# Kernel optimization log

Measured on AMD Instinct MI355X. Metric: run time of the kernel, lower is better.

The kernel has to match this reference:

```python
import jax, jax.numpy as jnp
import numpy as np

NEG_SLOPE = 0.2


def setup_inputs() -> dict:
    key = jax.random.key(0)
    ks = jax.random.split(key, 12)
    Nm, Na, E, Din, H, D = 50000, 50000, 400000, 128, 8, 32
    return {
        "master_feats": jax.random.normal(ks[0], (Nm, Din), jnp.float32),
        "attn_feats0": jax.random.normal(ks[1], (Na, Din), jnp.float32),
        "attn_feats1": jax.random.normal(ks[2], (Na, Din), jnp.float32),
        "src0": jax.random.randint(ks[3], (E,), 0, Na, jnp.int32),
        "dst0": jax.random.randint(ks[4], (E,), 0, Nm, jnp.int32),
        "src1": jax.random.randint(ks[5], (E,), 0, Na, jnp.int32),
        "dst1": jax.random.randint(ks[6], (E,), 0, Nm, jnp.int32),
        "W_master": jax.random.normal(ks[7], (Din, H * D), jnp.float32) * 0.08,
        "W0": jax.random.normal(ks[8], (Din, H * D), jnp.float32) * 0.08,
        "W1": jax.random.normal(ks[9], (Din, H * D), jnp.float32) * 0.08,
        "attn_l": jax.random.normal(ks[10], (H, D), jnp.float32) * 0.1,
        "attn_r": jax.random.normal(ks[11], (H, D), jnp.float32) * 0.1,
    }


def reference(master_feats, attn_feats0, attn_feats1, src0, dst0, src1, dst1,
              W_master, W0, W1, attn_l, attn_r):
    Nm = master_feats.shape[0]
    H, D = attn_l.shape

    # Per-node-type linear projections (no bias) + attention logits.
    ft_m = (master_feats @ W_master).reshape(Nm, H, D)        # [Nm,H,D]
    er = jnp.einsum("nhd,hd->nh", ft_m, attn_r)               # [Nm,H]

    def proj(feats, W):
        ft = (feats @ W).reshape(feats.shape[0], H, D)
        el = jnp.einsum("nhd,hd->nh", ft, attn_l)
        return ft, el

    ft0, el0 = proj(attn_feats0, W0)
    ft1, el1 = proj(attn_feats1, W1)

    lrelu = lambda x: jnp.where(x >= 0, x, NEG_SLOPE * x)
    e0 = lrelu(el0[src0] + er[dst0])                          # [E0,H]
    e1 = lrelu(el1[src1] + er[dst1])                          # [E1,H]

    # Heterograph edge softmax: normalize over ALL incoming edges of each
    # master node, regardless of source node type (subtract dst-max for
    # stability; mathematically identical to the conditional path in source).
    dst = jnp.concatenate([dst0, dst1])
    e = jnp.concatenate([e0, e1], axis=0)                     # [E0+E1,H]
    emax = jax.ops.segment_max(e, dst, num_segments=Nm)
    emax = jnp.where(jnp.isfinite(emax), emax, 0.0)           # nodes w/o edges
    ee = jnp.exp(e - emax[dst])
    esum = jax.ops.segment_sum(ee, dst, num_segments=Nm)
    a = ee / esum[dst]                                        # [E0+E1,H]

    # u_mul_e + sum aggregation onto master nodes.
    E0 = src0.shape[0]
    msg = jnp.concatenate(
        [ft0[src0] * a[:E0, :, None], ft1[src1] * a[E0:, :, None]], axis=0
    )                                                         # [E,H,D]
    rst = jax.ops.segment_sum(msg, dst, num_segments=Nm)      # [Nm,H,D]
    return rst
```

## Files before the change

kernel.cpp:

```cpp
#include <hip/hip_runtime.h>
#include <cstdint>
#include <cstddef>

#define NEG_SLOPE 0.2f

typedef __attribute__((ext_vector_type(8))) short short8;
typedef __attribute__((ext_vector_type(4))) float f32x4;

static __device__ __forceinline__ unsigned short f2bf(float x) {
  uint32_t u = __float_as_uint(x);
  uint32_t r = (u + 0x7FFFu + ((u >> 16) & 1u)) >> 16;
  return (unsigned short)r;
}
static __device__ __forceinline__ float bf2f(unsigned short b) {
  return __uint_as_float(((uint32_t)b) << 16);
}

__global__ void wt_kernel(const float* __restrict__ W0, const float* __restrict__ W1,
                          const float* __restrict__ W2,
                          unsigned short* __restrict__ T0, unsigned short* __restrict__ T1,
                          unsigned short* __restrict__ T2) {
  const float* W = (blockIdx.y == 0) ? W0 : (blockIdx.y == 1) ? W1 : W2;
  unsigned short* T = (blockIdx.y == 0) ? T0 : (blockIdx.y == 1) ? T1 : T2;
  int c = blockIdx.x * 2 + (threadIdx.x >> 7);
  int k = threadIdx.x & 127;
  T[c * 128 + k] = f2bf(W[k * 256 + c]);
}

__global__ __launch_bounds__(256)
void proj_mfma_kernel(const float* __restrict__ fm, const float* __restrict__ fa0,
                      const float* __restrict__ fa1,
                      const unsigned short* __restrict__ Wtm,
                      const unsigned short* __restrict__ Wt0,
                      const unsigned short* __restrict__ Wt1,
                      const float* __restrict__ attn_l, const float* __restrict__ attn_r,
                      int Nm, int Na0, int Na1,
                      unsigned short* __restrict__ ft_all, float* __restrict__ el_all,
                      float* __restrict__ er) {
  const int z = blockIdx.z;
  const float* feats = (z == 0) ? fm : (z == 1) ? fa0 : fa1;
  const unsigned short* Wt = (z == 0) ? Wtm : (z == 1) ? Wt0 : Wt1;
  const float* av = (z == 0) ? attn_r : attn_l;
  const int N = (z == 0) ? Nm : (z == 1) ? Na0 : Na1;
  unsigned short* ft_out = (z == 0) ? nullptr
                         : (z == 1) ? ft_all : ft_all + (size_t)Na0 * 256;
  float* el_out = (z == 0) ? er : (z == 1) ? el_all : el_all + (size_t)Na0 * 8;

  const int rb = blockIdx.x * 64;
  if (rb >= N) return;

  __shared__ unsigned short As[64 * 128];
  const int t = threadIdx.x;
  const int wid = t >> 6, lane = t & 63;
  const int l15 = lane & 15, l4 = lane >> 4;
  const int cbw = wid * 64;
  const int head0 = cbw >> 5;

  short8 bf[4][4];
  #pragma unroll
  for (int nf = 0; nf < 4; ++nf) {
    const unsigned short* wp = &Wt[(size_t)(cbw + nf * 16 + l15) * 128];
    #pragma unroll
    for (int kb = 0; kb < 4; ++kb)
      bf[kb][nf] = *(const short8*)(wp + kb * 32 + l4 * 8);
  }

  #pragma unroll
  for (int it = 0; it < 8; ++it) {
    int i = it * 256 + t;
    int r = i >> 5, kc = (i & 31) << 2;
    float4 f = make_float4(0.f, 0.f, 0.f, 0.f);
    if (rb + r < N) f = *(const float4*)(&feats[(size_t)(rb + r) * 128 + kc]);
    ushort4 u;
    u.x = f2bf(f.x); u.y = f2bf(f.y); u.z = f2bf(f.z); u.w = f2bf(f.w);
    uint32_t byte = ((uint32_t)(r * 256 + kc * 2)) ^ ((uint32_t)((r & 7) << 4));
    *(ushort4*)((char*)As + byte) = u;
  }
  __syncthreads();

  f32x4 acc[4][4];
  #pragma unroll
  for (int a = 0; a < 4; ++a)
    #pragma unroll
    for (int b = 0; b < 4; ++b)
      acc[a][b] = (f32x4){0.f, 0.f, 0.f, 0.f};

  #pragma unroll
  for (int kb = 0; kb < 4; ++kb) {
    short8 af[4];
    #pragma unroll
    for (int mf = 0; mf < 4; ++mf) {
      int row = mf * 16 + l15;
      uint32_t byte = ((uint32_t)(row * 256 + kb * 64 + l4 * 16)) ^ ((uint32_t)((row & 7) << 4));
      af[mf] = *(const short8*)((const char*)As + byte);
    }
    #pragma unroll
    for (int mf = 0; mf < 4; ++mf)
      #pragma unroll
      for (int nf = 0; nf < 4; ++nf)
        acc[mf][nf] = __builtin_amdgcn_mfma_f32_16x16x32_bf16(
            bf[kb][nf], af[mf], acc[mf][nf], 0, 0, 0);
  }

  float avf[4][4];
  #pragma unroll
  for (int nf = 0; nf < 4; ++nf)
    #pragma unroll
    for (int reg = 0; reg < 4; ++reg)
      avf[nf][reg] = av[(head0 + (nf >> 1)) * 32 + (nf & 1) * 16 + l4 * 4 + reg];

  #pragma unroll
  for (int mf = 0; mf < 4; ++mf) {
    int node = rb + mf * 16 + l15;
    bool ok = node < N;
    if (ft_out != nullptr && ok) {
      size_t base = (size_t)node * 256 + cbw + l4 * 4;
      #pragma unroll
      for (int nf = 0; nf < 4; ++nf) {
        ushort4 u;
        u.x = f2bf(acc[mf][nf][0]); u.y = f2bf(acc[mf][nf][1]);
        u.z = f2bf(acc[mf][nf][2]); u.w = f2bf(acc[mf][nf][3]);
        *(ushort4*)(&ft_out[base + nf * 16]) = u;
      }
    }
    #pragma unroll
    for (int hh = 0; hh < 2; ++hh) {
      float p = 0.f;
      #pragma unroll
      for (int reg = 0; reg < 4; ++reg) {
        p = fmaf(acc[mf][2 * hh][reg], avf[2 * hh][reg], p);
        p = fmaf(acc[mf][2 * hh + 1][reg], avf[2 * hh + 1][reg], p);
      }
      p += __shfl_xor(p, 16);
      p += __shfl_xor(p, 32);
      if (ok && l4 == 0)
        el_out[(size_t)node * 8 + head0 + hh] = p;
    }
  }
}

__global__ void count_deg_kernel(const int* __restrict__ dst0, int E0,
                                 const int* __restrict__ dst1, int E1,
                                 int* __restrict__ deg) {
  int E = E0 + E1;
  for (int i = blockIdx.x * blockDim.x + threadIdx.x; i < E;
       i += gridDim.x * blockDim.x) {
    int d = (i < E0) ? dst0[i] : dst1[i - E0];
    atomicAdd(&deg[d], 1);
  }
}

__global__ __launch_bounds__(1024)
void block_reduce_kernel(const int* __restrict__ deg, int* __restrict__ partial, int n) {
  __shared__ int wsum[16];
  const int t = threadIdx.x;
  int idx = blockIdx.x * 1024 + t;
  int v = (idx < n) ? deg[idx] : 0;
  #pragma unroll
  for (int off = 1; off < 64; off <<= 1) v += __shfl_xor(v, off);
  if ((t & 63) == 0) wsum[t >> 6] = v;
  __syncthreads();
  if (t < 16) {
    int x = wsum[t];
    #pragma unroll
    for (int off = 1; off < 16; off <<= 1) x += __shfl_xor(x, off);
    if (t == 0) partial[blockIdx.x] = x;
  }
}

__global__ __launch_bounds__(64)
void partial_scan_kernel(const int* __restrict__ partial, int* __restrict__ base,
                         int nb, int* __restrict__ offs, int n) {
  const int t = threadIdx.x;
  int v = (t < nb) ? partial[t] : 0;
  int incl = v;
  #pragma unroll
  for (int off = 1; off < 64; off <<= 1) {
    int x = __shfl_up(incl, off);
    if (t >= off) incl += x;
  }
  if (t < nb) base[t] = incl - v;
  if (t == nb - 1) offs[n] = incl;
}

__global__ __launch_bounds__(1024)
void apply_scan_kernel(const int* __restrict__ deg, const int* __restrict__ base,
                       int* __restrict__ offs, int* __restrict__ cursor, int n) {
  __shared__ int wsum[16];
  const int t = threadIdx.x;
  const int idx = blockIdx.x * 1024 + t;
  int v = (idx < n) ? deg[idx] : 0;
  const int lane = t & 63, w = t >> 6;
  int incl = v;
  #pragma unroll
  for (int off = 1; off < 64; off <<= 1) {
    int x = __shfl_up(incl, off);
    if (lane >= off) incl += x;
  }
  if (lane == 63) wsum[w] = incl;
  __syncthreads();
  if (t < 16) {
    int x = wsum[t];
    #pragma unroll
    for (int off = 1; off < 16; off <<= 1) {
      int y = __shfl_up(x, off);
      if (t >= off) x += y;
    }
    wsum[t] = x;
  }
  __syncthreads();
  int excl = base[blockIdx.x] + ((w > 0) ? wsum[w - 1] : 0) + incl - v;
  if (idx < n) {
    offs[idx] = excl;
    cursor[idx] = excl;
  }
}

__global__ void scatter_kernel(const int* __restrict__ src0, const int* __restrict__ dst0, int E0,
                               const int* __restrict__ src1, const int* __restrict__ dst1, int E1,
                               int* __restrict__ cursor, char* __restrict__ recs,
                               const float* __restrict__ el, const float* __restrict__ er,
                               int Na0) {
  int E = E0 + E1;
  for (int i = blockIdx.x * blockDim.x + threadIdx.x; i < E;
       i += gridDim.x * blockDim.x) {
    int s, d;
    if (i < E0) { s = src0[i]; d = dst0[i]; }
    else        { s = src1[i - E0] + Na0; d = dst1[i - E0]; }
    int pos = atomicAdd(&cursor[d], 1);

    const float* elp = &el[(size_t)s * 8];
    const float* erp = &er[(size_t)d * 8];
    float4 ea = *(const float4*)elp, eb = *(const float4*)(elp + 4);
    float4 ra = *(const float4*)erp, rb = *(const float4*)(erp + 4);
    float w[8];
    w[0] = ea.x + ra.x; w[1] = ea.y + ra.y; w[2] = ea.z + ra.z; w[3] = ea.w + ra.w;
    w[4] = eb.x + rb.x; w[5] = eb.y + rb.y; w[6] = eb.z + rb.z; w[7] = eb.w + rb.w;
    uint32_t pk[4];
    #pragma unroll
    for (int q = 0; q < 4; ++q) {
      float v0 = w[2 * q], v1 = w[2 * q + 1];
      v0 = fmaxf(v0, NEG_SLOPE * v0);
      v1 = fmaxf(v1, NEG_SLOPE * v1);
      uint32_t b0 = f2bf(__expf(v0)), b1 = f2bf(__expf(v1));
      pk[q] = b0 | (b1 << 16);
    }
    char* rp = recs + ((size_t)(uint32_t)pos << 5);
    *(uint4*)rp = make_uint4((uint32_t)s, pk[0], pk[1], pk[2]);
    *(uint32_t*)(rp + 16) = pk[3];
  }
}

__global__ __launch_bounds__(256)
void aggregate_kernel(const int* __restrict__ offs, const char* __restrict__ recs,
                      const unsigned short* __restrict__ ft,
                      float* __restrict__ rst, int Nm) {
  int gid = blockIdx.x * blockDim.x + threadIdx.x;
  int n = gid >> 6;
  int lane = threadIdx.x & 63;
  if (n >= Nm) return;
  const int nu = __builtin_amdgcn_readfirstlane(n);
  const int beg = offs[nu], end = offs[nu + 1];
  const int h = lane >> 3;
  const char* ftl = (const char*)ft + lane * 8;
  float o0 = 0.f, o1 = 0.f, o2 = 0.f, o3 = 0.f;
  float sw = 0.f;

  #pragma unroll 8
  for (int i = beg; i < end; ++i) {
    const uint32_t* rp = (const uint32_t*)(recs + ((size_t)(uint32_t)i << 5));
    uint32_t sct = rp[0];
    uint32_t d0 = rp[1], d1 = rp[2], d2 = rp[3], d3 = rp[4];
    uint2 g = *(const uint2*)(ftl + ((size_t)sct << 9));
    uint32_t wa = (h & 2) ? d1 : d0;
    uint32_t wb = (h & 2) ? d3 : d2;
    uint32_t wsl = (h & 4) ? wb : wa;
    float w = __uint_as_float((h & 1) ? (wsl & 0xffff0000u) : (wsl << 16));
    sw += w;
    o0 = fmaf(w, __uint_as_float(g.x << 16), o0);
    o1 = fmaf(w, __uint_as_float(g.x & 0xffff0000u), o1);
    o2 = fmaf(w, __uint_as_float(g.y << 16), o2);
    o3 = fmaf(w, __uint_as_float(g.y & 0xffff0000u), o3);
  }

  if (beg < end) {
    float inv = 1.0f / sw;
    o0 *= inv; o1 *= inv; o2 *= inv; o3 *= inv;
  }
  *(float4*)(&rst[(size_t)n * 256 + lane * 4]) = make_float4(o0, o1, o2, o3);
}

extern "C" void kernel_launch(void* const* d_in, const int* in_sizes, int n_in,
                              void* d_out, int out_size, void* d_ws, size_t ws_size,
                              hipStream_t stream) {
  const float* master = (const float*)d_in[0];
  const float* af0    = (const float*)d_in[1];
  const float* af1    = (const float*)d_in[2];
  const int*   src0   = (const int*)d_in[3];
  const int*   dst0   = (const int*)d_in[4];
  const int*   src1   = (const int*)d_in[5];
  const int*   dst1   = (const int*)d_in[6];
  const float* Wm     = (const float*)d_in[7];
  const float* W0     = (const float*)d_in[8];
  const float* W1     = (const float*)d_in[9];
  const float* attn_l = (const float*)d_in[10];
  const float* attn_r = (const float*)d_in[11];

  const int Nm  = in_sizes[0] / 128;
  const int Na0 = in_sizes[1] / 128;
  const int Na1 = in_sizes[2] / 128;
  const int E0  = in_sizes[3];
  const int E1  = in_sizes[5];
  float* rst = (float*)d_out;

  char* ws = (char*)d_ws;
  size_t off = 0;
  auto alloc = [&](size_t b) -> char* {
    char* p = ws + off;
    off += (b + 511) & ~(size_t)511;
    return p;
  };
  unsigned short* ft = (unsigned short*)alloc((size_t)(Na0 + Na1) * 256 * sizeof(unsigned short));
  float* el = (float*)alloc((size_t)(Na0 + Na1) * 8 * sizeof(float));
  float* er = (float*)alloc((size_t)Nm * 8 * sizeof(float));
  unsigned short* Wtm = (unsigned short*)alloc(256 * 128 * sizeof(unsigned short));
  unsigned short* Wt0 = (unsigned short*)alloc(256 * 128 * sizeof(unsigned short));
  unsigned short* Wt1 = (unsigned short*)alloc(256 * 128 * sizeof(unsigned short));
  int* deg     = (int*)alloc((size_t)Nm * sizeof(int));
  int* offs    = (int*)alloc((size_t)(Nm + 1) * sizeof(int));
  int* cursor  = (int*)alloc((size_t)Nm * sizeof(int));
  int* partial = (int*)alloc(64 * sizeof(int));
  int* pbase   = (int*)alloc(64 * sizeof(int));
  char* recs   = alloc((size_t)(E0 + E1) * 32);

  wt_kernel<<<dim3(128, 3), 256, 0, stream>>>(Wm, W0, W1, Wtm, Wt0, Wt1);

  int Nmax = Nm > Na0 ? Nm : Na0; if (Na1 > Nmax) Nmax = Na1;
  const int mb = (Nmax + 63) / 64;
  proj_mfma_kernel<<<dim3(mb, 1, 3), 256, 0, stream>>>(
      master, af0, af1, Wtm, Wt0, Wt1, attn_l, attn_r,
      Nm, Na0, Na1, ft, el, er);

  hipMemsetAsync(deg, 0, (size_t)Nm * sizeof(int), stream);
  const int E = E0 + E1;
  const int eb = (E + 255) / 256;
  count_deg_kernel<<<eb, 256, 0, stream>>>(dst0, E0, dst1, E1, deg);
  const int nb = (Nm + 1023) / 1024;
  block_reduce_kernel<<<nb, 1024, 0, stream>>>(deg, partial, Nm);
  partial_scan_kernel<<<1, 64, 0, stream>>>(partial, pbase, nb, offs, Nm);
  apply_scan_kernel<<<nb, 1024, 0, stream>>>(deg, pbase, offs, cursor, Nm);
  scatter_kernel<<<eb, 256, 0, stream>>>(src0, dst0, E0, src1, dst1, E1,
                                         cursor, recs, el, er, Na0);

  aggregate_kernel<<<(Nm + 3) / 4, 256, 0, stream>>>(offs, recs, ft, rst, Nm);
}
```

Baseline: 205.9 us.

## Fold W_master and attn_r into a 128x8 matrix for er computation

Computes er directly as master_feats @ (W_master·attn_r), with the small 128x8 product precomputed by qk_kernel and applied by a dedicated fp32 er_kernel. This removes the full 128x256 MFMA projection of master nodes, which was only ever used to produce attention logits. The ft and rst stores also become nontemporal to reduce cache pollution. The change adds two extra small launches and alters rounding, since er is now computed fully in fp32 rather than from bf16 MFMA inputs.

Measured after the change: 214.6 us. 4.2% more time.

```diff
diff --git a/kernel.cpp b/kernel.cpp
--- a/kernel.cpp
+++ b/kernel.cpp
@@ -6,45 +6,96 @@
 
 typedef __attribute__((ext_vector_type(8))) short short8;
 typedef __attribute__((ext_vector_type(4))) float f32x4;
+typedef __attribute__((ext_vector_type(4))) unsigned short u16x4;
 
 static __device__ __forceinline__ unsigned short f2bf(float x) {
   uint32_t u = __float_as_uint(x);
   uint32_t r = (u + 0x7FFFu + ((u >> 16) & 1u)) >> 16;
   return (unsigned short)r;
 }
-static __device__ __forceinline__ float bf2f(unsigned short b) {
-  return __uint_as_float(((uint32_t)b) << 16);
-}
 
 __global__ void wt_kernel(const float* __restrict__ W0, const float* __restrict__ W1,
-                          const float* __restrict__ W2,
-                          unsigned short* __restrict__ T0, unsigned short* __restrict__ T1,
-                          unsigned short* __restrict__ T2) {
-  const float* W = (blockIdx.y == 0) ? W0 : (blockIdx.y == 1) ? W1 : W2;
-  unsigned short* T = (blockIdx.y == 0) ? T0 : (blockIdx.y == 1) ? T1 : T2;
+                          unsigned short* __restrict__ T0, unsigned short* __restrict__ T1) {
+  const float* W = (blockIdx.y == 0) ? W0 : W1;
+  unsigned short* T = (blockIdx.y == 0) ? T0 : T1;
   int c = blockIdx.x * 2 + (threadIdx.x >> 7);
   int k = threadIdx.x & 127;
   T[c * 128 + k] = f2bf(W[k * 256 + c]);
 }
 
+__global__ __launch_bounds__(1024)
+void qk_kernel(const float* __restrict__ Wm, const float* __restrict__ ar,
+               float* __restrict__ Q) {
+  int t = threadIdx.x;
+  int k = t >> 3, h = t & 7;
+  const float* wr = &Wm[k * 256 + h * 32];
+  const float* av = &ar[h * 32];
+  float s = 0.f;
+  #pragma unroll
+  for (int q = 0; q < 8; ++q) {
+    float4 w4 = *(const float4*)(wr + q * 4);
+    float4 a4 = *(const float4*)(av + q * 4);
+    s += w4.x * a4.x + w4.y * a4.y + w4.z * a4.z + w4.w * a4.w;
+  }
+  Q[h * 128 + k] = s;
+}
+
 __global__ __launch_bounds__(256)
-void proj_mfma_kernel(const float* __restrict__ fm, const float* __restrict__ fa0,
-                      const float* __restrict__ fa1,
-                      const unsigned short* __restrict__ Wtm,
+void er_kernel(const float* __restrict__ feats, const float* __restrict__ Q,
+               float* __restrict__ er, int N) {
+  __shared__ float Qs[8 * 128];
+  const int t = threadIdx.x;
+  ((float4*)Qs)[t] = ((const float4*)Q)[t];
+  __syncthreads();
+
+  const int lane = t & 63, wave = t >> 6;
+  const int j = lane & 7;
+  const int n = blockIdx.x * 32 + wave * 8 + (lane >> 3);
+  const bool ok = n < N;
+
+  float acc[8] = {};
+  #pragma unroll
+  for (int q = 0; q < 4; ++q) {
+    float4 f = make_float4(0.f, 0.f, 0.f, 0.f);
+    int kc = q * 32 + j * 4;
+    if (ok) f = *(const float4*)(&feats[(size_t)n * 128 + kc]);
+    #pragma unroll
+    for (int h = 0; h < 8; ++h) {
+      const float* qr = &Qs[h * 128 + kc];
+      acc[h] = fmaf(f.x, qr[0], acc[h]);
+      acc[h] = fmaf(f.y, qr[1], acc[h]);
+      acc[h] = fmaf(f.z, qr[2], acc[h]);
+      acc[h] = fmaf(f.w, qr[3], acc[h]);
+    }
+  }
+  #pragma unroll
+  for (int h = 0; h < 8; ++h) {
+    acc[h] += __shfl_xor(acc[h], 1);
+    acc[h] += __shfl_xor(acc[h], 2);
+    acc[h] += __shfl_xor(acc[h], 4);
+  }
+  float out = acc[0];
+  out = (j == 1) ? acc[1] : out;  out = (j == 2) ? acc[2] : out;
+  out = (j == 3) ? acc[3] : out;  out = (j == 4) ? acc[4] : out;
+  out = (j == 5) ? acc[5] : out;  out = (j == 6) ? acc[6] : out;
+  out = (j == 7) ? acc[7] : out;
+  if (ok) er[(size_t)n * 8 + j] = out;
+}
+
+__global__ __launch_bounds__(256)
+void proj_mfma_kernel(const float* __restrict__ fa0, const float* __restrict__ fa1,
                       const unsigned short* __restrict__ Wt0,
                       const unsigned short* __restrict__ Wt1,
-                      const float* __restrict__ attn_l, const float* __restrict__ attn_r,
-                      int Nm, int Na0, int Na1,
-                      unsigned short* __restrict__ ft_all, float* __restrict__ el_all,
-                      float* __restrict__ er) {
+                      const float* __restrict__ attn_l,
+                      int Na0, int Na1,
+                      unsigned short* __restrict__ ft_all, float* __restrict__ el_all) {
   const int z = blockIdx.z;
-  const float* feats = (z == 0) ? fm : (z == 1) ? fa0 : fa1;
-  const unsigned short* Wt = (z == 0) ? Wtm : (z == 1) ? Wt0 : Wt1;
-  const float* av = (z == 0) ? attn_r : attn_l;
-  const int N = (z == 0) ? Nm : (z == 1) ? Na0 : Na1;
-  unsigned short* ft_out = (z == 0) ? nullptr
-                         : (z == 1) ? ft_all : ft_all + (size_t)Na0 * 256;
-  float* el_out = (z == 0) ? er : (z == 1) ? el_all : el_all + (size_t)Na0 * 8;
+  const float* feats = (z == 0) ? fa0 : fa1;
+  const unsigned short* Wt = (z == 0) ? Wt0 : Wt1;
+  const float* av = attn_l;
+  const int N = (z == 0) ? Na0 : Na1;
+  unsigned short* ft_out = (z == 0) ? ft_all : ft_all + (size_t)Na0 * 256;
+  float* el_out = (z == 0) ? el_all : el_all + (size_t)Na0 * 8;
 
   const int rb = blockIdx.x * 64;
   if (rb >= N) return;
@@ -113,14 +164,14 @@
   for (int mf = 0; mf < 4; ++mf) {
     int node = rb + mf * 16 + l15;
     bool ok = node < N;
-    if (ft_out != nullptr && ok) {
+    if (ok) {
       size_t base = (size_t)node * 256 + cbw + l4 * 4;
       #pragma unroll
       for (int nf = 0; nf < 4; ++nf) {
-        ushort4 u;
+        u16x4 u;
         u.x = f2bf(acc[mf][nf][0]); u.y = f2bf(acc[mf][nf][1]);
         u.z = f2bf(acc[mf][nf][2]); u.w = f2bf(acc[mf][nf][3]);
-        *(ushort4*)(&ft_out[base + nf * 16]) = u;
+        __builtin_nontemporal_store(u, (u16x4*)(&ft_out[base + nf * 16]));
       }
     }
     #pragma unroll
@@ -287,7 +338,8 @@
     float inv = 1.0f / sw;
     o0 *= inv; o1 *= inv; o2 *= inv; o3 *= inv;
   }
-  *(float4*)(&rst[(size_t)n * 256 + lane * 4]) = make_float4(o0, o1, o2, o3);
+  f32x4 o = {o0, o1, o2, o3};
+  __builtin_nontemporal_store(o, (f32x4*)(&rst[(size_t)n * 256 + lane * 4]));
 }
 
 extern "C" void kernel_launch(void* const* d_in, const int* in_sizes, int n_in,
@@ -323,9 +375,9 @@
   unsigned short* ft = (unsigned short*)alloc((size_t)(Na0 + Na1) * 256 * sizeof(unsigned short));
   float* el = (float*)alloc((size_t)(Na0 + Na1) * 8 * sizeof(float));
   float* er = (float*)alloc((size_t)Nm * 8 * sizeof(float));
-  unsigned short* Wtm = (unsigned short*)alloc(256 * 128 * sizeof(unsigned short));
   unsigned short* Wt0 = (unsigned short*)alloc(256 * 128 * sizeof(unsigned short));
   unsigned short* Wt1 = (unsigned short*)alloc(256 * 128 * sizeof(unsigned short));
+  float* Q     = (float*)alloc(8 * 128 * sizeof(float));
   int* deg     = (int*)alloc((size_t)Nm * sizeof(int));
   int* offs    = (int*)alloc((size_t)(Nm + 1) * sizeof(int));
   int* cursor  = (int*)alloc((size_t)Nm * sizeof(int));
@@ -333,13 +385,14 @@
   int* pbase   = (int*)alloc(64 * sizeof(int));
   char* recs   = alloc((size_t)(E0 + E1) * 32);
 
-  wt_kernel<<<dim3(128, 3), 256, 0, stream>>>(Wm, W0, W1, Wtm, Wt0, Wt1);
-
-  int Nmax = Nm > Na0 ? Nm : Na0; if (Na1 > Nmax) Nmax = Na1;
+  wt_kernel<<<dim3(128, 2), 256, 0, stream>>>(W0, W1, Wt0, Wt1);
+  qk_kernel<<<1, 1024, 0, stream>>>(Wm, attn_r, Q);
+  er_kernel<<<(Nm + 31) / 32, 256, 0, stream>>>(master, Q, er, Nm);
+
+  int Nmax = Na0 > Na1 ? Na0 : Na1;
   const int mb = (Nmax + 63) / 64;
-  proj_mfma_kernel<<<dim3(mb, 1, 3), 256, 0, stream>>>(
-      master, af0, af1, Wtm, Wt0, Wt1, attn_l, attn_r,
-      Nm, Na0, Na1, ft, el, er);
+  proj_mfma_kernel<<<dim3(mb, 1, 2), 256, 0, stream>>>(
+      af0, af1, Wt0, Wt1, attn_l, Na0, Na1, ft, el);
 
   hipMemsetAsync(deg, 0, (size_t)Nm * sizeof(int), stream);
   const int E = E0 + E1;
```
